# Kernel tuning notes

Hardware: AMD Instinct MI355X
Metric: run time of the kernel (lower is better)

## Reference

```python
import jax, jax.numpy as jnp
import numpy as np

H = 8
D = 64  # head_dim = node_dim // num_heads = 512 // 8
NODE = 512
EPS = 1e-5


def setup_inputs() -> dict:
    key = jax.random.key(0)
    ks = jax.random.split(key, 8)
    S, IN = 4096, 1024
    return {
        "protT5_emb": jax.random.normal(ks[0], (S, IN), jnp.float32),
        "contact_matrix": jax.random.uniform(ks[1], (S, S), jnp.float32),
        "Wq": jax.random.normal(ks[2], (NODE, IN), jnp.float32) * 0.02,
        "bq": jnp.zeros((NODE,), jnp.float32),
        "Wk": jax.random.normal(ks[3], (NODE, IN), jnp.float32) * 0.02,
        "bk": jnp.zeros((NODE,), jnp.float32),
        "Wv": jax.random.normal(ks[4], (NODE, IN), jnp.float32) * 0.02,
        "bv": jnp.zeros((NODE,), jnp.float32),
        "Wc": jnp.ones((1, H, 1, 1), jnp.float32),
        "Wo": jax.random.normal(ks[5], (NODE, NODE), jnp.float32) * 0.02,
        "bo": jnp.zeros((NODE,), jnp.float32),
        "gamma": jnp.ones((NODE,), jnp.float32),
        "beta": jnp.zeros((NODE,), jnp.float32),
    }


def reference(protT5_emb, contact_matrix, Wq, bq, Wk, bk, Wv, bv, Wc, Wo, bo, gamma, beta):
    S = protT5_emb.shape[0]
    # QKV projections -> [H, S, D]
    Q = (protT5_emb @ Wq.T + bq).reshape(S, H, D).transpose(1, 0, 2)
    K = (protT5_emb @ Wk.T + bk).reshape(S, H, D).transpose(1, 0, 2)
    V = (protT5_emb @ Wv.T + bv).reshape(S, H, D).transpose(1, 0, 2)
    # raw scores [H, S, S]
    attn_raw = jnp.einsum('hsd,htd->hst', Q, K) / jnp.sqrt(jnp.float32(D))
    # multiplicative contact mask, per-head learnable scale
    contact_mask = contact_matrix[None, :, :] * Wc.reshape(H, 1, 1)
    attn_weight = jax.nn.softmax(attn_raw * contact_mask, axis=-1)
    attn_output = jnp.einsum('hst,htd->hsd', attn_weight, V)  # [H, S, D]
    # FAITHFUL to torch: transpose(0,1).view(S,-1) on [1,H,S,D] flattens in
    # (head, seq, dim) order -> scrambled [S, H*D] reshape, not head concat.
    attn_output = attn_output.reshape(S, H * D)
    aug = attn_output @ Wo.T + bo
    x = aug + protT5_emb[:, :NODE]
    mu = jnp.mean(x, axis=-1, keepdims=True)
    var = jnp.mean((x - mu) ** 2, axis=-1, keepdims=True)
    return (x - mu) * jax.lax.rsqrt(var + EPS) * gamma + beta
```

## Files before the change

### kernel.cpp

```cpp
#include <hip/hip_runtime.h>
#include <stdint.h>

#define SEQ 4096
#define INDIM 1024
#define NODEDIM 512
#define NH 8
#define HD 64
#define LSTR 72

typedef __bf16 bf16x8 __attribute__((ext_vector_type(8)));
typedef float f32x4 __attribute__((ext_vector_type(4)));

__device__ __forceinline__ unsigned short f2bf(float f) {
    union { float f; uint32_t u; } v; v.f = f;
    uint32_t u = v.u;
    uint32_t r = (u + 0x7fffu + ((u >> 16) & 1u)) >> 16;
    return (unsigned short)r;
}

__global__ __launch_bounds__(256) void cvt_kernel(const float* __restrict__ src,
                                                  unsigned short* __restrict__ dst, int n) {
    int i = (blockIdx.x * 256 + threadIdx.x) * 4;
    if (i < n) {
        float4 v = *(const float4*)(src + i);
        ushort4 o;
        o.x = f2bf(v.x); o.y = f2bf(v.y); o.z = f2bf(v.z); o.w = f2bf(v.w);
        *(ushort4*)(dst + i) = o;
    }
}

__global__ __launch_bounds__(256) void qkv_gemm(const unsigned short* __restrict__ A,
                                                const unsigned short* __restrict__ B,
                                                const float* __restrict__ bq,
                                                const float* __restrict__ bk,
                                                const float* __restrict__ bv,
                                                unsigned short* __restrict__ Qo,
                                                unsigned short* __restrict__ Ko,
                                                unsigned short* __restrict__ VTo) {
    __shared__ unsigned short As[128 * 32];
    __shared__ unsigned short Bs[128 * 32];
    __shared__ unsigned short Ts[128 * 40];
    const int tid = threadIdx.x;
    const int lane = tid & 63, wave = tid >> 6;
    const int wm = wave >> 1, wn = wave & 1;
    const int quad = lane >> 4, l16 = lane & 15;
    const int m0 = blockIdx.x * 128;
    const int n0 = blockIdx.y * 128;

    f32x4 acc[4][4] = {};

    for (int k0 = 0; k0 < INDIM; k0 += 32) {
        __syncthreads();
        for (int i = 0; i < 2; ++i) {
            int c = tid + 256 * i;
            int row = c >> 2, qq = c & 3;
            *(bf16x8*)&As[row * 32 + qq * 8] =
                *(const bf16x8*)(A + (size_t)(m0 + row) * INDIM + k0 + qq * 8);
            *(bf16x8*)&Bs[row * 32 + qq * 8] =
                *(const bf16x8*)(B + (size_t)(n0 + row) * INDIM + k0 + qq * 8);
        }
        __syncthreads();
        bf16x8 af[4], bf[4];
        for (int mi = 0; mi < 4; ++mi)
            af[mi] = *(const bf16x8*)&As[(wm * 64 + mi * 16 + l16) * 32 + quad * 8];
        for (int ni = 0; ni < 4; ++ni)
            bf[ni] = *(const bf16x8*)&Bs[(wn * 64 + ni * 16 + l16) * 32 + quad * 8];
        for (int mi = 0; mi < 4; ++mi)
            for (int ni = 0; ni < 4; ++ni)
                acc[mi][ni] = __builtin_amdgcn_mfma_f32_16x16x32_bf16(af[mi], bf[ni], acc[mi][ni], 0, 0, 0);
    }

    if (blockIdx.y < 8) {
        unsigned short* outp = (blockIdx.y < 4) ? Qo : Ko;
        const float* biasp = (blockIdx.y < 4) ? bq : bk;
        for (int mi = 0; mi < 4; ++mi)
            for (int ni = 0; ni < 4; ++ni)
                for (int r = 0; r < 4; ++r) {
                    int s = m0 + wm * 64 + mi * 16 + quad * 4 + r;
                    int n = n0 + wn * 64 + ni * 16 + l16;
                    int h = (n >> 6) & 7;
                    int dd = n & 63;
                    float v = acc[mi][ni][r] + biasp[n & 511];
                    outp[((size_t)h * SEQ + s) * HD + dd] = f2bf(v);
                }
    } else {
        for (int chunk = 0; chunk < 4; ++chunk) {
            const int cwm = chunk >> 1;
            const int milo = (chunk & 1) * 2;
            __syncthreads();
            if (wm == cwm) {
                for (int mi2 = 0; mi2 < 2; ++mi2) {
                    int mi = milo + mi2;
                    for (int ni = 0; ni < 4; ++ni) {
                        int ddf = wn * 64 + ni * 16 + l16;
                        float bias = bv[(n0 + ddf) & 511];
                        for (int r = 0; r < 4; ++r) {
                            int sl = mi2 * 16 + quad * 4 + r;
                            Ts[ddf * 40 + sl] = f2bf(acc[mi][ni][r] + bias);
                        }
                    }
                }
            }
            __syncthreads();
            for (int pass = 0; pass < 2; ++pass) {
                int c = pass * 256 + tid;
                int row = c >> 2, part = c & 3;
                int nfull = n0 + row;
                int h = (nfull >> 6) & 7, dd = nfull & 63;
                *(bf16x8*)(VTo + ((size_t)h * HD + dd) * SEQ + m0 + chunk * 32 + part * 8) =
                    *(const bf16x8*)&Ts[row * 40 + part * 8];
            }
        }
    }
}

__global__ __launch_bounds__(256, 4) void attn_kernel(const unsigned short* __restrict__ Q,
                                                      const unsigned short* __restrict__ K,
                                                      const unsigned short* __restrict__ VT,
                                                      const float* __restrict__ CM,
                                                      const float* __restrict__ Wc,
                                                      float* __restrict__ O0,
                                                      float* __restrict__ O1,
                                                      float* __restrict__ l0,
                                                      float* __restrict__ l1) {
    __shared__ unsigned short Qs[64 * LSTR];
    __shared__ unsigned short Ks[64 * LSTR];
    __shared__ unsigned short Vs[64 * LSTR];
    __shared__ unsigned short Ps[64 * LSTR];
    const int tid = threadIdx.x;
    const int lane = tid & 63, wave = tid >> 6;
    const int quad = lane >> 4, l16 = lane & 15;
    const int h = blockIdx.y;
    const int q0 = blockIdx.x * 64;
    const int split = blockIdx.z;
    float* __restrict__ Op = split ? O1 : O0;
    float* __restrict__ lp = split ? l1 : l0;
    const float wch = Wc[h] * 0.125f;

    for (int i = 0; i < 2; ++i) {
        int c = tid + 256 * i;
        int row = c >> 3, part = c & 7;
        bf16x8 v = *(const bf16x8*)(Q + ((size_t)h * SEQ + q0 + row) * HD + part * 8);
        for (int j = 0; j < 8; ++j) v[j] = (__bf16)((float)v[j] * wch);
        *(bf16x8*)&Qs[row * LSTR + part * 8] = v;
    }

    f32x4 O[4] = {};
    float l_part[4] = {0.f, 0.f, 0.f, 0.f};
    const float* cmbase = CM + (size_t)(q0 + wave * 16 + quad * 4) * SEQ + l16;

    const int tbeg = split * (SEQ / 2);
    for (int t0 = tbeg; t0 < tbeg + SEQ / 2; t0 += 64) {
        float cmv[4][4];
        for (int r = 0; r < 4; ++r)
            for (int nt = 0; nt < 4; ++nt)
                cmv[r][nt] = cmbase[(size_t)r * SEQ + t0 + nt * 16];

        __syncthreads();
        for (int i = 0; i < 2; ++i) {
            int c = tid + 256 * i;
            int row = c >> 3, part = c & 7;
            *(bf16x8*)&Ks[row * LSTR + part * 8] =
                *(const bf16x8*)(K + ((size_t)h * SEQ + t0 + row) * HD + part * 8);
            *(bf16x8*)&Vs[row * LSTR + part * 8] =
                *(const bf16x8*)(VT + ((size_t)h * HD + row) * SEQ + t0 + part * 8);
        }
        __syncthreads();

        bf16x8 a0 = *(const bf16x8*)&Qs[(wave * 16 + l16) * LSTR + quad * 8];
        bf16x8 a1 = *(const bf16x8*)&Qs[(wave * 16 + l16) * LSTR + 32 + quad * 8];
        f32x4 sc[4];
        for (int nt = 0; nt < 4; ++nt) {
            bf16x8 b0 = *(const bf16x8*)&Ks[(nt * 16 + l16) * LSTR + quad * 8];
            bf16x8 b1 = *(const bf16x8*)&Ks[(nt * 16 + l16) * LSTR + 32 + quad * 8];
            f32x4 z = {0.f, 0.f, 0.f, 0.f};
            z = __builtin_amdgcn_mfma_f32_16x16x32_bf16(a0, b0, z, 0, 0, 0);
            z = __builtin_amdgcn_mfma_f32_16x16x32_bf16(a1, b1, z, 0, 0, 0);
            sc[nt] = z;
        }

        for (int r = 0; r < 4; ++r) {
            for (int nt = 0; nt < 4; ++nt) {
                float pv = __expf(sc[nt][r] * cmv[r][nt]);
                l_part[r] += pv;
                Ps[(wave * 16 + quad * 4 + r) * LSTR + nt * 16 + l16] = f2bf(pv);
            }
        }

        asm volatile("s_waitcnt lgkmcnt(0)" ::: "memory");

        bf16x8 pa0 = *(const bf16x8*)&Ps[(wave * 16 + l16) * LSTR + quad * 8];
        bf16x8 pa1 = *(const bf16x8*)&Ps[(wave * 16 + l16) * LSTR + 32 + quad * 8];
        for (int nt = 0; nt < 4; ++nt) {
            bf16x8 vb0 = *(const bf16x8*)&Vs[(nt * 16 + l16) * LSTR + quad * 8];
            bf16x8 vb1 = *(const bf16x8*)&Vs[(nt * 16 + l16) * LSTR + 32 + quad * 8];
            f32x4 o = O[nt];
            o = __builtin_amdgcn_mfma_f32_16x16x32_bf16(pa0, vb0, o, 0, 0, 0);
            o = __builtin_amdgcn_mfma_f32_16x16x32_bf16(pa1, vb1, o, 0, 0, 0);
            O[nt] = o;
        }
    }

    for (int r = 0; r < 4; ++r) {
        float s = l_part[r];
        for (int off = 1; off < 16; off <<= 1) s += __shfl_xor(s, off);
        l_part[r] = s;
    }
    if (l16 == 0)
        for (int r = 0; r < 4; ++r)
            lp[(size_t)h * SEQ + q0 + wave * 16 + quad * 4 + r] = l_part[r];
    for (int nt = 0; nt < 4; ++nt)
        for (int r = 0; r < 4; ++r) {
            int sg = q0 + wave * 16 + quad * 4 + r;
            Op[((size_t)h * SEQ + sg) * HD + nt * 16 + l16] = O[nt][r];
        }
}

__global__ __launch_bounds__(256) void combine_kernel(const float* __restrict__ O0,
                                                      const float* __restrict__ O1,
                                                      const float* __restrict__ l0,
                                                      const float* __restrict__ l1,
                                                      unsigned short* __restrict__ AO) {
    int idx = blockIdx.x * 256 + threadIdx.x;
    int e = idx * 4;
    int row = e >> 6;
    float4 a = *(const float4*)(O0 + e);
    float4 b = *(const float4*)(O1 + e);
    float linv = 1.f / (l0[row] + l1[row]);
    ushort4 o;
    o.x = f2bf((a.x + b.x) * linv);
    o.y = f2bf((a.y + b.y) * linv);
    o.z = f2bf((a.z + b.z) * linv);
    o.w = f2bf((a.w + b.w) * linv);
    *(ushort4*)(AO + e) = o;
}

__global__ __launch_bounds__(256) void out_gemm(const unsigned short* __restrict__ A,
                                                const unsigned short* __restrict__ B,
                                                const float* __restrict__ bo,
                                                const float* __restrict__ emb,
                                                float* __restrict__ X) {
    __shared__ unsigned short As[128 * 32];
    __shared__ unsigned short Bs[128 * 32];
    const int tid = threadIdx.x;
    const int lane = tid & 63, wave = tid >> 6;
    const int wm = wave >> 1, wn = wave & 1;
    const int quad = lane >> 4, l16 = lane & 15;
    const int m0 = blockIdx.x * 128;
    const int n0 = blockIdx.y * 128;

    f32x4 acc[4][4] = {};

    for (int k0 = 0; k0 < NODEDIM; k0 += 32) {
        __syncthreads();
        for (int i = 0; i < 2; ++i) {
            int c = tid + 256 * i;
            int row = c >> 2, qq = c & 3;
            *(bf16x8*)&As[row * 32 + qq * 8] =
                *(const bf16x8*)(A + (size_t)(m0 + row) * NODEDIM + k0 + qq * 8);
            *(bf16x8*)&Bs[row * 32 + qq * 8] =
                *(const bf16x8*)(B + (size_t)(n0 + row) * NODEDIM + k0 + qq * 8);
        }
        __syncthreads();
        bf16x8 af[4], bf[4];
        for (int mi = 0; mi < 4; ++mi)
            af[mi] = *(const bf16x8*)&As[(wm * 64 + mi * 16 + l16) * 32 + quad * 8];
        for (int ni = 0; ni < 4; ++ni)
            bf[ni] = *(const bf16x8*)&Bs[(wn * 64 + ni * 16 + l16) * 32 + quad * 8];
        for (int mi = 0; mi < 4; ++mi)
            for (int ni = 0; ni < 4; ++ni)
                acc[mi][ni] = __builtin_amdgcn_mfma_f32_16x16x32_bf16(af[mi], bf[ni], acc[mi][ni], 0, 0, 0);
    }

    for (int mi = 0; mi < 4; ++mi)
        for (int ni = 0; ni < 4; ++ni)
            for (int r = 0; r < 4; ++r) {
                int s = m0 + wm * 64 + mi * 16 + quad * 4 + r;
                int n = n0 + wn * 64 + ni * 16 + l16;
                float v = acc[mi][ni][r] + bo[n] + emb[(size_t)s * INDIM + n];
                X[(size_t)s * NODEDIM + n] = v;
            }
}

__global__ __launch_bounds__(256) void ln_kernel(const float* __restrict__ X,
                                                 const float* __restrict__ gamma,
                                                 const float* __restrict__ beta,
                                                 float* __restrict__ out) {
    const int s = blockIdx.x;
    const int n = threadIdx.x * 2;
    float2 v = *(const float2*)&X[(size_t)s * NODEDIM + n];
    float sum = v.x + v.y;
    float sq = v.x * v.x + v.y * v.y;
    for (int off = 32; off > 0; off >>= 1) {
        sum += __shfl_down(sum, off);
        sq += __shfl_down(sq, off);
    }
    __shared__ float ssum[4], ssq[4];
    const int wave = threadIdx.x >> 6, lane = threadIdx.x & 63;
    if (lane == 0) { ssum[wave] = sum; ssq[wave] = sq; }
    __syncthreads();
    float tsum = ssum[0] + ssum[1] + ssum[2] + ssum[3];
    float tsq = ssq[0] + ssq[1] + ssq[2] + ssq[3];
    float mu = tsum * (1.f / 512.f);
    float var = tsq * (1.f / 512.f) - mu * mu;
    float rstd = rsqrtf(var + 1e-5f);
    float2 g = *(const float2*)&gamma[n];
    float2 b = *(const float2*)&beta[n];
    float2 o;
    o.x = (v.x - mu) * rstd * g.x + b.x;
    o.y = (v.y - mu) * rstd * g.y + b.y;
    *(float2*)&out[(size_t)s * NODEDIM + n] = o;
}

extern "C" void kernel_launch(void* const* d_in, const int* in_sizes, int n_in,
                              void* d_out, int out_size, void* d_ws, size_t ws_size,
                              hipStream_t stream) {
    const float* emb = (const float*)d_in[0];
    const float* cm  = (const float*)d_in[1];
    const float* Wq  = (const float*)d_in[2];
    const float* bq  = (const float*)d_in[3];
    const float* Wk  = (const float*)d_in[4];
    const float* bk  = (const float*)d_in[5];
    const float* Wv  = (const float*)d_in[6];
    const float* bv  = (const float*)d_in[7];
    const float* Wc  = (const float*)d_in[8];
    const float* Wo  = (const float*)d_in[9];
    const float* bo  = (const float*)d_in[10];
    const float* gamma = (const float*)d_in[11];
    const float* beta  = (const float*)d_in[12];
    float* out = (float*)d_out;

    unsigned short* ws = (unsigned short*)d_ws;
    unsigned short* emb_bf  = ws;
    unsigned short* wqkv_bf = emb_bf + 4194304;
    unsigned short* wo_bf   = wqkv_bf + 1572864;
    unsigned short* Qb  = wo_bf + 262144;
    unsigned short* Kb  = Qb + 2097152;
    unsigned short* VTb = Kb + 2097152;
    unsigned short* AOb = VTb + 2097152;
    float* X = (float*)(AOb + 2097152);
    float* O0 = (float*)emb_bf;
    float* O1 = X;
    float* l0 = (float*)wqkv_bf;
    float* l1 = l0 + NH * SEQ;

    cvt_kernel<<<4096, 256, 0, stream>>>(emb, emb_bf, 4194304);
    cvt_kernel<<<512, 256, 0, stream>>>(Wq, wqkv_bf, 524288);
    cvt_kernel<<<512, 256, 0, stream>>>(Wk, wqkv_bf + 524288, 524288);
    cvt_kernel<<<512, 256, 0, stream>>>(Wv, wqkv_bf + 1048576, 524288);
    cvt_kernel<<<256, 256, 0, stream>>>(Wo, wo_bf, 262144);

    qkv_gemm<<<dim3(32, 12), 256, 0, stream>>>(emb_bf, wqkv_bf, bq, bk, bv, Qb, Kb, VTb);
    attn_kernel<<<dim3(64, 8, 2), 256, 0, stream>>>(Qb, Kb, VTb, cm, Wc, O0, O1, l0, l1);
    combine_kernel<<<2048, 256, 0, stream>>>(O0, O1, l0, l1, AOb);
    out_gemm<<<dim3(32, 4), 256, 0, stream>>>(AOb, wo_bf, bo, emb, X);
    ln_kernel<<<4096, 256, 0, stream>>>(X, gamma, beta, out);
}
```

Before: 282.9 us.

## Fuse conversion launches, prefetch K/V in registers, exp2, smaller out_gemm tiles

Several changes land together. The five fp32-to-bf16 conversion launches become one kernel. The attention loop now prefetches the next K/V tile into registers so global loads overlap the MFMA work. Q and P share one shared-memory buffer, which cuts LDS use and may raise occupancy. Exp now uses the hardware exp2 instruction with log2e folded into the Q scale, and P is truncated to bf16 instead of rounded. out_gemm moves to 64-row tiles to launch twice as many blocks, and the truncation slightly reduces numerical accuracy.

```diff
diff --git a/kernel.cpp b/kernel.cpp
--- a/kernel.cpp
+++ b/kernel.cpp
@@ -18,15 +18,34 @@
     return (unsigned short)r;
 }
 
-__global__ __launch_bounds__(256) void cvt_kernel(const float* __restrict__ src,
-                                                  unsigned short* __restrict__ dst, int n) {
-    int i = (blockIdx.x * 256 + threadIdx.x) * 4;
-    if (i < n) {
-        float4 v = *(const float4*)(src + i);
-        ushort4 o;
-        o.x = f2bf(v.x); o.y = f2bf(v.y); o.z = f2bf(v.z); o.w = f2bf(v.w);
-        *(ushort4*)(dst + i) = o;
-    }
+__device__ __forceinline__ float fast_exp2(float x) {
+    float r;
+    asm volatile("v_exp_f32 %0, %1" : "=v"(r) : "v"(x));
+    return r;
+}
+
+__global__ __launch_bounds__(256) void cvt_all(const float* __restrict__ emb,
+                                               const float* __restrict__ Wq,
+                                               const float* __restrict__ Wk,
+                                               const float* __restrict__ Wv,
+                                               const float* __restrict__ Wo,
+                                               unsigned short* __restrict__ demb,
+                                               unsigned short* __restrict__ dwqkv,
+                                               unsigned short* __restrict__ dwo) {
+    int b = blockIdx.x;
+    const float* src;
+    unsigned short* dst;
+    int off;
+    if (b < 4096)      { src = emb; dst = demb;            off = b; }
+    else if (b < 4608) { src = Wq;  dst = dwqkv;           off = b - 4096; }
+    else if (b < 5120) { src = Wk;  dst = dwqkv + 524288;  off = b - 4608; }
+    else if (b < 5632) { src = Wv;  dst = dwqkv + 1048576; off = b - 5120; }
+    else               { src = Wo;  dst = dwo;             off = b - 5632; }
+    int i = (off * 256 + threadIdx.x) * 4;
+    float4 v = *(const float4*)(src + i);
+    ushort4 o;
+    o.x = f2bf(v.x); o.y = f2bf(v.y); o.z = f2bf(v.z); o.w = f2bf(v.w);
+    *(ushort4*)(dst + i) = o;
 }
 
 __global__ __launch_bounds__(256) void qkv_gemm(const unsigned short* __restrict__ A,
@@ -123,10 +142,9 @@
                                                       float* __restrict__ O1,
                                                       float* __restrict__ l0,
                                                       float* __restrict__ l1) {
-    __shared__ unsigned short Qs[64 * LSTR];
+    __shared__ unsigned short QPs[64 * LSTR];
     __shared__ unsigned short Ks[64 * LSTR];
     __shared__ unsigned short Vs[64 * LSTR];
-    __shared__ unsigned short Ps[64 * LSTR];
     const int tid = threadIdx.x;
     const int lane = tid & 63, wave = tid >> 6;
     const int quad = lane >> 4, l16 = lane & 15;
@@ -135,40 +153,62 @@
     const int split = blockIdx.z;
     float* __restrict__ Op = split ? O1 : O0;
     float* __restrict__ lp = split ? l1 : l0;
-    const float wch = Wc[h] * 0.125f;
-
-    for (int i = 0; i < 2; ++i) {
-        int c = tid + 256 * i;
-        int row = c >> 3, part = c & 7;
-        bf16x8 v = *(const bf16x8*)(Q + ((size_t)h * SEQ + q0 + row) * HD + part * 8);
-        for (int j = 0; j < 8; ++j) v[j] = (__bf16)((float)v[j] * wch);
-        *(bf16x8*)&Qs[row * LSTR + part * 8] = v;
-    }
+    const float wch = Wc[h] * 0.125f * 1.44269504f;
+
+    const int srow0 = tid >> 3, spart = tid & 7;
+    const int srow1 = (tid + 256) >> 3;
+
+    {
+        bf16x8 v0 = *(const bf16x8*)(Q + ((size_t)h * SEQ + q0 + srow0) * HD + spart * 8);
+        bf16x8 v1 = *(const bf16x8*)(Q + ((size_t)h * SEQ + q0 + srow1) * HD + spart * 8);
+        for (int j = 0; j < 8; ++j) {
+            v0[j] = (__bf16)((float)v0[j] * wch);
+            v1[j] = (__bf16)((float)v1[j] * wch);
+        }
+        *(bf16x8*)&QPs[srow0 * LSTR + spart * 8] = v0;
+        *(bf16x8*)&QPs[srow1 * LSTR + spart * 8] = v1;
+    }
+
+    const int tbeg = split * (SEQ / 2);
+    const int tend = tbeg + SEQ / 2;
+
+    const unsigned short* kp0 = K + ((size_t)h * SEQ + tbeg + srow0) * HD + spart * 8;
+    const unsigned short* kp1 = K + ((size_t)h * SEQ + tbeg + srow1) * HD + spart * 8;
+    const unsigned short* vp0 = VT + ((size_t)h * HD + srow0) * SEQ + tbeg + spart * 8;
+    const unsigned short* vp1 = VT + ((size_t)h * HD + srow1) * SEQ + tbeg + spart * 8;
+    bf16x8 kr0 = *(const bf16x8*)kp0;
+    bf16x8 kr1 = *(const bf16x8*)kp1;
+    bf16x8 vr0 = *(const bf16x8*)vp0;
+    bf16x8 vr1 = *(const bf16x8*)vp1;
+
+    __syncthreads();
+    bf16x8 a0 = *(const bf16x8*)&QPs[(wave * 16 + l16) * LSTR + quad * 8];
+    bf16x8 a1 = *(const bf16x8*)&QPs[(wave * 16 + l16) * LSTR + 32 + quad * 8];
 
     f32x4 O[4] = {};
     float l_part[4] = {0.f, 0.f, 0.f, 0.f};
     const float* cmbase = CM + (size_t)(q0 + wave * 16 + quad * 4) * SEQ + l16;
 
-    const int tbeg = split * (SEQ / 2);
-    for (int t0 = tbeg; t0 < tbeg + SEQ / 2; t0 += 64) {
+    for (int t0 = tbeg; t0 < tend; t0 += 64) {
         float cmv[4][4];
         for (int r = 0; r < 4; ++r)
             for (int nt = 0; nt < 4; ++nt)
                 cmv[r][nt] = cmbase[(size_t)r * SEQ + t0 + nt * 16];
 
         __syncthreads();
-        for (int i = 0; i < 2; ++i) {
-            int c = tid + 256 * i;
-            int row = c >> 3, part = c & 7;
-            *(bf16x8*)&Ks[row * LSTR + part * 8] =
-                *(const bf16x8*)(K + ((size_t)h * SEQ + t0 + row) * HD + part * 8);
-            *(bf16x8*)&Vs[row * LSTR + part * 8] =
-                *(const bf16x8*)(VT + ((size_t)h * HD + row) * SEQ + t0 + part * 8);
-        }
-        __syncthreads();
-
-        bf16x8 a0 = *(const bf16x8*)&Qs[(wave * 16 + l16) * LSTR + quad * 8];
-        bf16x8 a1 = *(const bf16x8*)&Qs[(wave * 16 + l16) * LSTR + 32 + quad * 8];
+        *(bf16x8*)&Ks[srow0 * LSTR + spart * 8] = kr0;
+        *(bf16x8*)&Ks[srow1 * LSTR + spart * 8] = kr1;
+        *(bf16x8*)&Vs[srow0 * LSTR + spart * 8] = vr0;
+        *(bf16x8*)&Vs[srow1 * LSTR + spart * 8] = vr1;
+        __syncthreads();
+
+        if (t0 + 64 < tend) {
+            kr0 = *(const bf16x8*)(kp0 + (size_t)(t0 + 64 - tbeg) * HD);
+            kr1 = *(const bf16x8*)(kp1 + (size_t)(t0 + 64 - tbeg) * HD);
+            vr0 = *(const bf16x8*)(vp0 + (t0 + 64 - tbeg));
+            vr1 = *(const bf16x8*)(vp1 + (t0 + 64 - tbeg));
+        }
+
         f32x4 sc[4];
         for (int nt = 0; nt < 4; ++nt) {
             bf16x8 b0 = *(const bf16x8*)&Ks[(nt * 16 + l16) * LSTR + quad * 8];
@@ -181,16 +221,18 @@
 
         for (int r = 0; r < 4; ++r) {
             for (int nt = 0; nt < 4; ++nt) {
-                float pv = __expf(sc[nt][r] * cmv[r][nt]);
+                float pv = fast_exp2(sc[nt][r] * cmv[r][nt]);
                 l_part[r] += pv;
-                Ps[(wave * 16 + quad * 4 + r) * LSTR + nt * 16 + l16] = f2bf(pv);
+                union { float f; uint32_t u; } pu; pu.f = pv;
+                QPs[(wave * 16 + quad * 4 + r) * LSTR + nt * 16 + l16] =
+                    (unsigned short)(pu.u >> 16);
             }
         }
 
         asm volatile("s_waitcnt lgkmcnt(0)" ::: "memory");
 
-        bf16x8 pa0 = *(const bf16x8*)&Ps[(wave * 16 + l16) * LSTR + quad * 8];
-        bf16x8 pa1 = *(const bf16x8*)&Ps[(wave * 16 + l16) * LSTR + 32 + quad * 8];
+        bf16x8 pa0 = *(const bf16x8*)&QPs[(wave * 16 + l16) * LSTR + quad * 8];
+        bf16x8 pa1 = *(const bf16x8*)&QPs[(wave * 16 + l16) * LSTR + 32 + quad * 8];
         for (int nt = 0; nt < 4; ++nt) {
             bf16x8 vb0 = *(const bf16x8*)&Vs[(nt * 16 + l16) * LSTR + quad * 8];
             bf16x8 vb1 = *(const bf16x8*)&Vs[(nt * 16 + l16) * LSTR + 32 + quad * 8];
@@ -240,46 +282,44 @@
                                                 const float* __restrict__ bo,
                                                 const float* __restrict__ emb,
                                                 float* __restrict__ X) {
-    __shared__ unsigned short As[128 * 32];
+    __shared__ unsigned short As[64 * 32];
     __shared__ unsigned short Bs[128 * 32];
     const int tid = threadIdx.x;
     const int lane = tid & 63, wave = tid >> 6;
-    const int wm = wave >> 1, wn = wave & 1;
     const int quad = lane >> 4, l16 = lane & 15;
-    const int m0 = blockIdx.x * 128;
+    const int m0 = blockIdx.x * 64;
     const int n0 = blockIdx.y * 128;
 
-    f32x4 acc[4][4] = {};
+    f32x4 acc[8] = {};
 
     for (int k0 = 0; k0 < NODEDIM; k0 += 32) {
         __syncthreads();
+        {
+            int row = tid >> 2, qq = tid & 3;
+            *(bf16x8*)&As[row * 32 + qq * 8] =
+                *(const bf16x8*)(A + (size_t)(m0 + row) * NODEDIM + k0 + qq * 8);
+        }
         for (int i = 0; i < 2; ++i) {
             int c = tid + 256 * i;
             int row = c >> 2, qq = c & 3;
-            *(bf16x8*)&As[row * 32 + qq * 8] =
-                *(const bf16x8*)(A + (size_t)(m0 + row) * NODEDIM + k0 + qq * 8);
             *(bf16x8*)&Bs[row * 32 + qq * 8] =
                 *(const bf16x8*)(B + (size_t)(n0 + row) * NODEDIM + k0 + qq * 8);
         }
         __syncthreads();
-        bf16x8 af[4], bf[4];
-        for (int mi = 0; mi < 4; ++mi)
-            af[mi] = *(const bf16x8*)&As[(wm * 64 + mi * 16 + l16) * 32 + quad * 8];
-        for (int ni = 0; ni < 4; ++ni)
-            bf[ni] = *(const bf16x8*)&Bs[(wn * 64 + ni * 16 + l16) * 32 + quad * 8];
-        for (int mi = 0; mi < 4; ++mi)
-            for (int ni = 0; ni < 4; ++ni)
-                acc[mi][ni] = __builtin_amdgcn_mfma_f32_16x16x32_bf16(af[mi], bf[ni], acc[mi][ni], 0, 0, 0);
-    }
-
-    for (int mi = 0; mi < 4; ++mi)
-        for (int ni = 0; ni < 4; ++ni)
-            for (int r = 0; r < 4; ++r) {
-                int s = m0 + wm * 64 + mi * 16 + quad * 4 + r;
-                int n = n0 + wn * 64 + ni * 16 + l16;
-                float v = acc[mi][ni][r] + bo[n] + emb[(size_t)s * INDIM + n];
-                X[(size_t)s * NODEDIM + n] = v;
-            }
+        bf16x8 af = *(const bf16x8*)&As[(wave * 16 + l16) * 32 + quad * 8];
+        for (int ni = 0; ni < 8; ++ni) {
+            bf16x8 bf = *(const bf16x8*)&Bs[(ni * 16 + l16) * 32 + quad * 8];
+            acc[ni] = __builtin_amdgcn_mfma_f32_16x16x32_bf16(af, bf, acc[ni], 0, 0, 0);
+        }
+    }
+
+    for (int ni = 0; ni < 8; ++ni)
+        for (int r = 0; r < 4; ++r) {
+            int s = m0 + wave * 16 + quad * 4 + r;
+            int n = n0 + ni * 16 + l16;
+            float v = acc[ni][r] + bo[n] + emb[(size_t)s * INDIM + n];
+            X[(size_t)s * NODEDIM + n] = v;
+        }
 }
 
 __global__ __launch_bounds__(256) void ln_kernel(const float* __restrict__ X,
@@ -344,15 +384,11 @@
     float* l0 = (float*)wqkv_bf;
     float* l1 = l0 + NH * SEQ;
 
-    cvt_kernel<<<4096, 256, 0, stream>>>(emb, emb_bf, 4194304);
-    cvt_kernel<<<512, 256, 0, stream>>>(Wq, wqkv_bf, 524288);
-    cvt_kernel<<<512, 256, 0, stream>>>(Wk, wqkv_bf + 524288, 524288);
-    cvt_kernel<<<512, 256, 0, stream>>>(Wv, wqkv_bf + 1048576, 524288);
-    cvt_kernel<<<256, 256, 0, stream>>>(Wo, wo_bf, 262144);
+    cvt_all<<<5888, 256, 0, stream>>>(emb, Wq, Wk, Wv, Wo, emb_bf, wqkv_bf, wo_bf);
 
     qkv_gemm<<<dim3(32, 12), 256, 0, stream>>>(emb_bf, wqkv_bf, bq, bk, bv, Qb, Kb, VTb);
     attn_kernel<<<dim3(64, 8, 2), 256, 0, stream>>>(Qb, Kb, VTb, cm, Wc, O0, O1, l0, l1);
     combine_kernel<<<2048, 256, 0, stream>>>(O0, O1, l0, l1, AOb);
-    out_gemm<<<dim3(32, 4), 256, 0, stream>>>(AOb, wo_bf, bo, emb, X);
+    out_gemm<<<dim3(64, 4), 256, 0, stream>>>(AOb, wo_bf, bo, emb, X);
     ln_kernel<<<4096, 256, 0, stream>>>(X, gamma, beta, out);
 }
```

After: 260.3 us. -8.0%, faster.
